# Kernel tuning notes

Measured on AMD Instinct MI355X. Metric: run time of the kernel, lower is better.

## Reference

```python
import math
import jax, jax.numpy as jnp
import numpy as np

STRATEGY = 'small'
K_PEAKS = 2
BW = math.radians(15.0)
HIGH_RATIO = 0.3
LOW_RATIO = 0.2
ALPHA = 1.2
BETA = 0.8
N_BINS = 180


def setup_inputs() -> dict:
    key = jax.random.key(0)
    k1, k2, k3 = jax.random.split(key, 3)
    x = jax.random.normal(k1, (16, 256, 128, 128), dtype=jnp.float32)
    w_in = jax.random.normal(k2, (16, 256), dtype=jnp.float32) * 0.06    # proj_in 1x1 conv weight [c_mid, C]
    w_out = jax.random.normal(k3, (256, 16), dtype=jnp.float32) * 0.25   # proj_out 1x1 conv weight [C, c_mid]
    return {"x": x, "w_in": w_in, "w_out": w_out}


def _forward(x, w_in, w_out):
    B, C, H, W = x.shape
    pi = jnp.float32(math.pi)
    cy, cx = H // 2, W // 2
    y = jnp.arange(H, dtype=jnp.float32)[:, None]
    xg = jnp.arange(W, dtype=jnp.float32)[None, :]
    r = jnp.sqrt((y - cy) ** 2 + (xg - cx) ** 2)                 # [H, W]
    theta = jnp.arctan2(y - cy, xg - cx) + pi                    # [H, W] in [0, 2pi]
    r_max = float(min(cy, cx))

    # 1x1 conv in
    x_proj = jnp.einsum('mc,bchw->bmhw', w_in, x)                # [B, c_mid, H, W]

    fs = jnp.fft.fftshift(jnp.fft.fft2(x_proj, norm='ortho'), axes=(-2, -1))
    mag = jnp.abs(fs)                                            # [B, c_mid, H, W]

    # ---- peak direction detection (180-bin angular histogram of high-freq energy) ----
    theta_mod = theta % pi
    high_mask = (r > HIGH_RATIO * r_max).astype(jnp.float32)     # [H, W]
    bin_edges = jnp.linspace(0.0, math.pi, N_BINS + 1, dtype=jnp.float32)
    mag_avg = mag.mean(axis=1)                                   # [B, H, W]
    weighted = (mag_avg * high_mask).reshape(B, -1)              # [B, H*W]
    bin_idx = jnp.clip(jnp.searchsorted(bin_edges, theta_mod.reshape(-1), side='left') - 1, 0, N_BINS - 1)
    energy = jax.vmap(lambda w: jax.ops.segment_sum(w, bin_idx, num_segments=N_BINS))(weighted)  # [B, 180]

    # smooth with [0.25, 0.5, 0.25], zero padding
    ep = jnp.pad(energy, ((0, 0), (1, 1)))
    es = 0.25 * ep[:, :-2] + 0.5 * ep[:, 1:-1] + 0.25 * ep[:, 2:]  # [B, 180]

    mean_e = es.mean(axis=-1, keepdims=True)
    is_peak = (es > mean_e) & (es > jnp.roll(es, 1, axis=-1)) & (es > jnp.roll(es, -1, axis=-1))
    vals = jnp.where(is_peak, es, -jnp.inf)
    topv, topi = jax.lax.top_k(vals, K_PEAKS)                    # [B, k]
    count = jnp.sum(topv > -jnp.inf, axis=-1)                    # [B] number of valid peaks (<= k)
    amax = jnp.argmax(es, axis=-1)                               # fallback when no peak found
    topi = jnp.where((count > 0)[:, None], topi, amax[:, None])
    eff = jnp.maximum(count, 1)
    pos = jnp.minimum(jnp.arange(K_PEAKS)[None, :], (eff - 1)[:, None])  # pad with last valid peak
    final_idx = jnp.take_along_axis(topi, pos, axis=1)           # [B, k]
    bin_center = (bin_edges[:-1] + bin_edges[1:]) * 0.5
    peak_angles = bin_center[final_idx]                          # [B, k]

    # ---- gain map (channel-independent) ----
    if STRATEGY == 'small':
        pa = peak_angles
        base_mask = high_mask
    else:
        pa = (peak_angles + pi / 2) % pi
        base_mask = (r <= LOW_RATIO * r_max).astype(jnp.float32)
    diff = jnp.abs(theta[None, None] - pa[:, :, None, None])     # [B, k, H, W]
    diff = jnp.minimum(diff, pi - diff)
    in_region = (diff <= BW) & (base_mask[None, None] > 0)
    enh = jnp.any(in_region, axis=1).astype(jnp.float32)         # [B, H, W]
    gain = jnp.where(enh > 0, jnp.float32(ALPHA), jnp.float32(1.0))
    other_high = high_mask[None] * (1.0 - enh)
    gain = gain * (1.0 - other_high) + other_high * BETA         # [B, H, W]

    fs_enh = fs * gain[:, None, :, :]
    x_enh = jnp.fft.ifft2(jnp.fft.ifftshift(fs_enh, axes=(-2, -1)), norm='ortho').real
    out = jnp.einsum('cm,bmhw->bchw', w_out, x_enh)
    return x + out


def reference(x, w_in, w_out):
    return _forward(x, w_in, w_out)
```

## Files before the change

kernel.cpp:

```cpp
#include <hip/hip_runtime.h>
#include <math.h>

#define NPX 16384

static constexpr float  PI_F   = 3.14159265358979323846f;
static constexpr double PI_D   = 3.14159265358979323846;
static constexpr double STEP_D = PI_D / 180.0;
static constexpr double BW_D   = 15.0 * (PI_D / 180.0);

typedef float f4 __attribute__((ext_vector_type(4)));
typedef float f2 __attribute__((ext_vector_type(2)));

__device__ __forceinline__ int swz(int r, int c) {
    return (r << 7) | (c ^ (r ^ (r >> 1)));
}
__device__ __forceinline__ int brev7(int x) { return (int)(__brev((unsigned)x) >> 25); }
__device__ __forceinline__ float2 cadd(float2 a, float2 b){ return make_float2(a.x+b.x, a.y+b.y); }
__device__ __forceinline__ float2 csub(float2 a, float2 b){ return make_float2(a.x-b.x, a.y-b.y); }
__device__ __forceinline__ float2 cmul(float2 a, float re, float im){
    return make_float2(a.x*re - a.y*im, a.x*im + a.y*re);
}
__device__ __forceinline__ double edge_d(int i) {
    return (i >= 180) ? PI_D : (double)i * STEP_D;
}

__global__ void k0_tables(double* __restrict__ theta_s, int* __restrict__ bin_s,
                          double* __restrict__ energy) {
    int p = blockIdx.x * blockDim.x + threadIdx.x;
    if (p < NPX) {
        int r = p >> 7, c = p & 127;
        int pix = ((brev7(r) ^ 64) << 7) | (brev7(c) ^ 64);
        int h = pix >> 7, w = pix & 127;
        double dy = (double)(h - 64), dx = (double)(w - 64);
        double theta = atan2(dy, dx) + PI_D;
        theta_s[p] = theta;
        double v = fmod(theta, PI_D);
        int cnt = 0;
        for (int i = 0; i <= 180; ++i) cnt += (edge_d(i) < v) ? 1 : 0;
        int bin = cnt - 1;
        if (bin < 0) bin = 0;
        if (bin > 179) bin = 179;
        int r2 = (h - 64)*(h - 64) + (w - 64)*(w - 64);
        bool high = (r2 >= 369);
        bin_s[p] = high ? bin : -1;
    }
    if (blockIdx.x == 0) {
        for (int i = threadIdx.x; i < 16 * 180; i += blockDim.x) energy[i] = 0.0;
    }
}

__global__ __launch_bounds__(256, 1) void k1_proj(const float* __restrict__ x,
        const float* __restrict__ w_in, float* __restrict__ xpp) {
    int b = blockIdx.y, z = blockIdx.z;
    int t4 = blockIdx.x * blockDim.x + threadIdx.x;
    const f4* xb = (const f4*)(x + ((size_t)b * 256 + (size_t)z * 128) * NPX);
    f4 acc[16];
    #pragma unroll
    for (int m = 0; m < 16; ++m) acc[m] = (f4)0.0f;
    #pragma unroll 16
    for (int c = 0; c < 128; ++c) {
        f4 xv = xb[(size_t)c * (NPX/4) + t4];
        #pragma unroll
        for (int m = 0; m < 16; ++m) {
            float wv = w_in[m * 256 + z * 128 + c];
            acc[m] += wv * xv;
        }
    }
    f4* xp = (f4*)xpp + ((size_t)z * 256 + b * 16) * (NPX/4);
    #pragma unroll
    for (int m = 0; m < 16; ++m) xp[(size_t)m * (NPX/4) + t4] = acc[m];
}

__global__ __launch_bounds__(1024) void k_fft_fwd(const float* __restrict__ xpp,
        float2* __restrict__ fs, const int* __restrict__ bin_s,
        double* __restrict__ energy) {
    extern __shared__ float2 lds[];
    __shared__ float twr[64], twi[64];
    __shared__ double histp[8][180];
    const int tid = threadIdx.x;
    const int img = blockIdx.x;
    if (tid < 64) {
        float ang = (float)tid * (PI_F / 64.0f);
        twr[tid] = cosf(ang);
        twi[tid] = sinf(ang);
    }
    if (tid < 180) {
        #pragma unroll
        for (int g = 0; g < 8; ++g) histp[g][tid] = 0.0;
    }
    const f4* s0 = (const f4*)xpp + (size_t)img * (NPX/4);
    const f4* s1 = (const f4*)xpp + (size_t)(256 + img) * (NPX/4);
    #pragma unroll
    for (int it = 0; it < 4; ++it) {
        int p4 = tid + it * 1024;
        f4 v = s0[p4] + s1[p4];
        int pb = p4 * 4;
        #pragma unroll
        for (int j = 0; j < 4; ++j) {
            int p = pb + j;
            lds[swz(p >> 7, p & 127)] = make_float2(v[j], 0.0f);
        }
    }
    __syncthreads();
    #pragma unroll
    for (int dim = 0; dim < 2; ++dim) {
        #pragma unroll
        for (int s = 0; s <= 4; s += 2) {
            const int q = 32 >> s;
            #pragma unroll
            for (int it = 0; it < 4; ++it) {
                int fb = tid + it * 1024;
                int o = fb & 127;
                int bfi = fb >> 7;
                int p = bfi & (q - 1);
                int g = bfi >> (5 - s);
                int P = g * (128 >> s) + p;
                int k1 = p << s;
                float tc = twr[k1],   ts = twi[k1];
                float uc = twr[2*k1], us = twi[2*k1];
                int e0, e1, e2, e3;
                if (dim == 0) { e0=swz(o,P); e1=swz(o,P+q); e2=swz(o,P+2*q); e3=swz(o,P+3*q); }
                else          { e0=swz(P,o); e1=swz(P+q,o); e2=swz(P+2*q,o); e3=swz(P+3*q,o); }
                float2 a = lds[e0], b = lds[e1], c = lds[e2], d = lds[e3];
                float2 u0 = cadd(a, c);
                float2 u1 = cmul(csub(a, c), tc, -ts);
                float2 v0 = cadd(b, d);
                float2 v1 = cmul(csub(b, d), -ts, -tc);
                lds[e0] = cadd(u0, v0);
                lds[e1] = cmul(csub(u0, v0), uc, -us);
                lds[e2] = cadd(u1, v1);
                lds[e3] = cmul(csub(u1, v1), uc, -us);
            }
            __syncthreads();
        }
        #pragma unroll
        for (int it = 0; it < 8; ++it) {
            int fb = tid + it * 1024;
            int o = fb & 127;
            int g = fb >> 7;
            int e0, e1;
            if (dim == 0) { e0 = swz(o, 2*g); e1 = swz(o, 2*g+1); }
            else          { e0 = swz(2*g, o); e1 = swz(2*g+1, o); }
            float2 a = lds[e0], b = lds[e1];
            lds[e0] = cadd(a, b);
            lds[e1] = csub(a, b);
        }
        __syncthreads();
    }
    float2* dst = fs + (size_t)img * NPX;
    const int bofs = (img >> 4) * 180;
    const int grp = tid >> 7;
    #pragma unroll
    for (int it = 0; it < 16; ++it) {
        int p = tid + it * 1024;
        int r = p >> 7, c = p & 127;
        float2 v = lds[swz(r, c)];
        dst[p] = v;
        int bh = bin_s[p];
        if (bh >= 0) {
            double m = sqrt((double)v.x * (double)v.x + (double)v.y * (double)v.y);
            atomicAdd(&histp[grp][bh], m);
        }
    }
    __syncthreads();
    if (tid < 180) {
        double s = 0.0;
        #pragma unroll
        for (int g = 0; g < 8; ++g) s += histp[g][tid];
        atomicAdd(&energy[bofs + tid], s);
    }
}

__global__ void k3_peaks(const double* __restrict__ energy, const double* __restrict__ theta_s,
                         const int* __restrict__ bin_s, float* __restrict__ gain_s) {
    __shared__ double e[180], es[180];
    __shared__ double pa[2];
    int b = blockIdx.x, tid = threadIdx.x;
    if (tid < 180) e[tid] = energy[b * 180 + tid];
    __syncthreads();
    if (tid < 180) {
        double l = (tid > 0)   ? e[tid-1] : 0.0;
        double r = (tid < 179) ? e[tid+1] : 0.0;
        es[tid] = 0.25*l + 0.5*e[tid] + 0.25*r;
    }
    __syncthreads();
    if (tid == 0) {
        double sum = 0.0;
        for (int i = 0; i < 180; ++i) sum += es[i];
        double mean = sum / 180.0;
        double v0 = -INFINITY, v1 = -INFINITY;
        int   i0 = -1, i1 = -1;
        for (int i = 0; i < 180; ++i) {
            double prev = es[(i + 179) % 180];
            double nxt  = es[(i + 1) % 180];
            bool pk = (es[i] > mean) && (es[i] > prev) && (es[i] > nxt);
            if (pk) {
                double v = es[i];
                if (v > v0)      { v1 = v0; i1 = i0; v0 = v; i0 = i; }
                else if (v > v1) { v1 = v;  i1 = i; }
            }
        }
        int idx0, idx1;
        if (i0 < 0) {
            double mv = es[0]; int mi = 0;
            for (int i = 1; i < 180; ++i) if (es[i] > mv) { mv = es[i]; mi = i; }
            idx0 = idx1 = mi;
        } else if (i1 < 0) { idx0 = idx1 = i0; }
        else               { idx0 = i0; idx1 = i1; }
        pa[0] = (edge_d(idx0) + edge_d(idx0 + 1)) * 0.5;
        pa[1] = (edge_d(idx1) + edge_d(idx1 + 1)) * 0.5;
    }
    __syncthreads();
    double pa0 = pa[0], pa1 = pa[1];
    for (int p = tid; p < NPX; p += blockDim.x) {
        double th = theta_s[p];
        bool high = bin_s[p] >= 0;
        double d0 = fabs(th - pa0); d0 = fmin(d0, PI_D - d0);
        double d1 = fabs(th - pa1); d1 = fmin(d1, PI_D - d1);
        bool enh = ((d0 <= BW_D) || (d1 <= BW_D)) && high;
        float g = enh ? 1.2f : (high ? 0.8f : 1.0f);
        gain_s[(size_t)b * NPX + p] = g * (1.0f / 16384.0f);
    }
}

__global__ __launch_bounds__(1024) void k_fft_inv(const float2* __restrict__ fs,
        const float* __restrict__ gain_s, float* __restrict__ xe) {
    extern __shared__ float2 lds[];
    __shared__ float twr[64], twi[64];
    const int tid = threadIdx.x;
    const int img = blockIdx.x;
    if (tid < 64) {
        float ang = (float)tid * (PI_F / 64.0f);
        twr[tid] = cosf(ang);
        twi[tid] = sinf(ang);
    }
    const f4* srcv = (const f4*)(fs + (size_t)img * NPX);
    const f2* gbv  = (const f2*)(gain_s + (size_t)(img >> 4) * NPX);
    #pragma unroll
    for (int it = 0; it < 8; ++it) {
        int q = tid + it * 1024;
        f4 v = srcv[q];
        f2 g = gbv[q];
        int p = q * 2;
        lds[swz(p >> 7, p & 127)]             = make_float2(v.x * g.x, v.y * g.x);
        lds[swz((p+1) >> 7, (p+1) & 127)]     = make_float2(v.z * g.y, v.w * g.y);
    }
    __syncthreads();
    #pragma unroll
    for (int dim = 0; dim < 2; ++dim) {
        #pragma unroll
        for (int it = 0; it < 8; ++it) {
            int fb = tid + it * 1024;
            int o = fb & 127;
            int g = fb >> 7;
            int e0, e1;
            if (dim == 0) { e0 = swz(o, 2*g); e1 = swz(o, 2*g+1); }
            else          { e0 = swz(2*g, o); e1 = swz(2*g+1, o); }
            float2 a = lds[e0], b = lds[e1];
            lds[e0] = cadd(a, b);
            lds[e1] = csub(a, b);
        }
        __syncthreads();
        #pragma unroll
        for (int s = 4; s >= 0; s -= 2) {
            const int q = 32 >> s;
            #pragma unroll
            for (int it = 0; it < 4; ++it) {
                int fb = tid + it * 1024;
                int o = fb & 127;
                int bfi = fb >> 7;
                int p = bfi & (q - 1);
                int g = bfi >> (5 - s);
                int P = g * (128 >> s) + p;
                int k1 = p << s;
                float tc = twr[k1],   ts = twi[k1];
                float uc = twr[2*k1], us = twi[2*k1];
                int e0, e1, e2, e3;
                if (dim == 0) { e0=swz(o,P); e1=swz(o,P+q); e2=swz(o,P+2*q); e3=swz(o,P+3*q); }
                else          { e0=swz(P,o); e1=swz(P+q,o); e2=swz(P+2*q,o); e3=swz(P+3*q,o); }
                float2 o0 = lds[e0], o1 = lds[e1], o2 = lds[e2], o3 = lds[e3];
                float2 t1 = cmul(o1, uc, us);
                float2 u0 = cadd(o0, t1);
                float2 v0 = csub(o0, t1);
                float2 t3 = cmul(o3, uc, us);
                float2 u1 = cadd(o2, t3);
                float2 v1 = csub(o2, t3);
                float2 ta = cmul(u1, tc, ts);
                float2 tb = cmul(v1, -ts, tc);
                lds[e0] = cadd(u0, ta);
                lds[e2] = csub(u0, ta);
                lds[e1] = cadd(v0, tb);
                lds[e3] = csub(v0, tb);
            }
            __syncthreads();
        }
    }
    float* dstx = xe + (size_t)img * NPX;
    #pragma unroll
    for (int it = 0; it < 16; ++it) {
        int p = tid + it * 1024;
        dstx[p] = lds[swz(p >> 7, p & 127)].x;
    }
}

__global__ __launch_bounds__(256, 1) void k5_out(const float* __restrict__ x,
        const float* __restrict__ w_out, const float* __restrict__ xe,
        float* __restrict__ out) {
    int b = blockIdx.z, ct = blockIdx.y, pt = blockIdx.x, t = threadIdx.x;
    int p4 = pt * 256 + t;
    const f4* xeb = (const f4*)(xe + (size_t)b * 16 * NPX);
    f4 xv[16];
    #pragma unroll
    for (int m = 0; m < 16; ++m) xv[m] = xeb[(size_t)m * (NPX/4) + p4];
    #pragma unroll 8
    for (int cc = 0; cc < 16; ++cc) {
        int c = ct * 16 + cc;
        size_t base = ((size_t)b * 256 + c) * NPX;
        f4 a = ((const f4*)(x + base))[p4];
        #pragma unroll
        for (int m = 0; m < 16; ++m) {
            float wv = w_out[c * 16 + m];
            a += wv * xv[m];
        }
        __builtin_nontemporal_store(a, (f4*)(out + base) + p4);
    }
}

extern "C" void kernel_launch(void* const* d_in, const int* in_sizes, int n_in,
                              void* d_out, int out_size, void* d_ws, size_t ws_size,
                              hipStream_t stream) {
    const float* x     = (const float*)d_in[0];
    const float* w_in  = (const float*)d_in[1];
    const float* w_out = (const float*)d_in[2];
    float* out = (float*)d_out;
    char* ws = (char*)d_ws;

    double* theta_s = (double*)(ws);
    int*    bin_s   = (int*)   (ws + 0x20000);
    double* energy  = (double*)(ws + 0x30000);
    float*  gain_s  = (float*) (ws + 0x40000);
    float*  xe      = (float*) (ws + 0x140000);
    float*  xpp = (float*)((char*)d_out + ((size_t)128 << 20));
    float2* fs  = (float2*)((char*)d_out + ((size_t)224 << 20));

    (void)hipFuncSetAttribute((const void*)k_fft_fwd,
            hipFuncAttributeMaxDynamicSharedMemorySize, 131072);
    (void)hipFuncSetAttribute((const void*)k_fft_inv,
            hipFuncAttributeMaxDynamicSharedMemorySize, 131072);

    k0_tables<<<dim3(64), dim3(256), 0, stream>>>(theta_s, bin_s, energy);
    k1_proj  <<<dim3(16, 16, 2), dim3(256), 0, stream>>>(x, w_in, xpp);
    k_fft_fwd<<<dim3(256), dim3(1024), 131072, stream>>>(xpp, fs, bin_s, energy);
    k3_peaks <<<dim3(16), dim3(256), 0, stream>>>(energy, theta_s, bin_s, gain_s);
    k_fft_inv<<<dim3(256), dim3(1024), 131072, stream>>>(fs, gain_s, xe);
    k5_out   <<<dim3(16, 16, 16), dim3(256), 0, stream>>>(x, w_out, xe, out);
}
```

Before: 253.3 us.

## Fuse forward FFT, peak detection and inverse FFT into one cooperative kernel

Merges the forward FFT, peak-finding/gain computation and inverse FFT into one cooperative kernel. A grid-wide sync after the histogram accumulation replaces the kernel boundary, and the spectrum stays in LDS, so the complex spectrum and gain map are no longer written to and read back from global memory. Each block recomputes the peaks for its batch redundantly. In exchange it relies on all 256 blocks of 1024 threads with 128KB LDS being co-resident, and it adds a grid barrier cost.

```diff
diff --git a/kernel.cpp b/kernel.cpp
--- a/kernel.cpp
+++ b/kernel.cpp
@@ -1,5 +1,8 @@
 #include <hip/hip_runtime.h>
+#include <hip/hip_cooperative_groups.h>
 #include <math.h>
+
+namespace cg = cooperative_groups;
 
 #define NPX 16384
 
@@ -71,12 +74,14 @@
     for (int m = 0; m < 16; ++m) xp[(size_t)m * (NPX/4) + t4] = acc[m];
 }
 
-__global__ __launch_bounds__(1024) void k_fft_fwd(const float* __restrict__ xpp,
-        float2* __restrict__ fs, const int* __restrict__ bin_s,
-        double* __restrict__ energy) {
+__global__ __launch_bounds__(1024) void k_fused(const float* __restrict__ xpp,
+        const int* __restrict__ bin_s, const double* __restrict__ theta_s,
+        double* __restrict__ energy, float* __restrict__ xe) {
     extern __shared__ float2 lds[];
     __shared__ float twr[64], twi[64];
     __shared__ double histp[8][180];
+    __shared__ double es[180];
+    __shared__ double pa[2];
     const int tid = threadIdx.x;
     const int img = blockIdx.x;
     if (tid < 64) {
@@ -147,15 +152,12 @@
         }
         __syncthreads();
     }
-    float2* dst = fs + (size_t)img * NPX;
     const int bofs = (img >> 4) * 180;
     const int grp = tid >> 7;
     #pragma unroll
     for (int it = 0; it < 16; ++it) {
         int p = tid + it * 1024;
-        int r = p >> 7, c = p & 127;
-        float2 v = lds[swz(r, c)];
-        dst[p] = v;
+        float2 v = lds[swz(p >> 7, p & 127)];
         int bh = bin_s[p];
         if (bh >= 0) {
             double m = sqrt((double)v.x * (double)v.x + (double)v.y * (double)v.y);
@@ -169,19 +171,13 @@
         for (int g = 0; g < 8; ++g) s += histp[g][tid];
         atomicAdd(&energy[bofs + tid], s);
     }
-}
-
-__global__ void k3_peaks(const double* __restrict__ energy, const double* __restrict__ theta_s,
-                         const int* __restrict__ bin_s, float* __restrict__ gain_s) {
-    __shared__ double e[180], es[180];
-    __shared__ double pa[2];
-    int b = blockIdx.x, tid = threadIdx.x;
-    if (tid < 180) e[tid] = energy[b * 180 + tid];
-    __syncthreads();
+    __threadfence();
+    cg::this_grid().sync();
     if (tid < 180) {
-        double l = (tid > 0)   ? e[tid-1] : 0.0;
-        double r = (tid < 179) ? e[tid+1] : 0.0;
-        es[tid] = 0.25*l + 0.5*e[tid] + 0.25*r;
+        int i = tid;
+        double l = (i > 0)   ? energy[bofs + i - 1] : 0.0;
+        double r = (i < 179) ? energy[bofs + i + 1] : 0.0;
+        es[i] = 0.25*l + 0.5*energy[bofs + i] + 0.25*r;
     }
     __syncthreads();
     if (tid == 0) {
@@ -212,38 +208,18 @@
     }
     __syncthreads();
     double pa0 = pa[0], pa1 = pa[1];
-    for (int p = tid; p < NPX; p += blockDim.x) {
+    #pragma unroll
+    for (int it = 0; it < 16; ++it) {
+        int p = tid + it * 1024;
         double th = theta_s[p];
         bool high = bin_s[p] >= 0;
         double d0 = fabs(th - pa0); d0 = fmin(d0, PI_D - d0);
         double d1 = fabs(th - pa1); d1 = fmin(d1, PI_D - d1);
         bool enh = ((d0 <= BW_D) || (d1 <= BW_D)) && high;
-        float g = enh ? 1.2f : (high ? 0.8f : 1.0f);
-        gain_s[(size_t)b * NPX + p] = g * (1.0f / 16384.0f);
-    }
-}
-
-__global__ __launch_bounds__(1024) void k_fft_inv(const float2* __restrict__ fs,
-        const float* __restrict__ gain_s, float* __restrict__ xe) {
-    extern __shared__ float2 lds[];
-    __shared__ float twr[64], twi[64];
-    const int tid = threadIdx.x;
-    const int img = blockIdx.x;
-    if (tid < 64) {
-        float ang = (float)tid * (PI_F / 64.0f);
-        twr[tid] = cosf(ang);
-        twi[tid] = sinf(ang);
-    }
-    const f4* srcv = (const f4*)(fs + (size_t)img * NPX);
-    const f2* gbv  = (const f2*)(gain_s + (size_t)(img >> 4) * NPX);
-    #pragma unroll
-    for (int it = 0; it < 8; ++it) {
-        int q = tid + it * 1024;
-        f4 v = srcv[q];
-        f2 g = gbv[q];
-        int p = q * 2;
-        lds[swz(p >> 7, p & 127)]             = make_float2(v.x * g.x, v.y * g.x);
-        lds[swz((p+1) >> 7, (p+1) & 127)]     = make_float2(v.z * g.y, v.w * g.y);
+        float g = (enh ? 1.2f : (high ? 0.8f : 1.0f)) * (1.0f / 16384.0f);
+        int e = swz(p >> 7, p & 127);
+        float2 v = lds[e];
+        lds[e] = make_float2(v.x * g, v.y * g);
     }
     __syncthreads();
     #pragma unroll
@@ -338,20 +314,19 @@
     double* theta_s = (double*)(ws);
     int*    bin_s   = (int*)   (ws + 0x20000);
     double* energy  = (double*)(ws + 0x30000);
-    float*  gain_s  = (float*) (ws + 0x40000);
     float*  xe      = (float*) (ws + 0x140000);
     float*  xpp = (float*)((char*)d_out + ((size_t)128 << 20));
-    float2* fs  = (float2*)((char*)d_out + ((size_t)224 << 20));
-
-    (void)hipFuncSetAttribute((const void*)k_fft_fwd,
-            hipFuncAttributeMaxDynamicSharedMemorySize, 131072);
-    (void)hipFuncSetAttribute((const void*)k_fft_inv,
+
+    (void)hipFuncSetAttribute((const void*)k_fused,
             hipFuncAttributeMaxDynamicSharedMemorySize, 131072);
 
     k0_tables<<<dim3(64), dim3(256), 0, stream>>>(theta_s, bin_s, energy);
     k1_proj  <<<dim3(16, 16, 2), dim3(256), 0, stream>>>(x, w_in, xpp);
-    k_fft_fwd<<<dim3(256), dim3(1024), 131072, stream>>>(xpp, fs, bin_s, energy);
-    k3_peaks <<<dim3(16), dim3(256), 0, stream>>>(energy, theta_s, bin_s, gain_s);
-    k_fft_inv<<<dim3(256), dim3(1024), 131072, stream>>>(fs, gain_s, xe);
+
+    void* args[] = { (void*)&xpp, (void*)&bin_s, (void*)&theta_s,
+                     (void*)&energy, (void*)&xe };
+    (void)hipLaunchCooperativeKernel((const void*)k_fused, dim3(256), dim3(1024),
+                                     args, 131072, stream);
+
     k5_out   <<<dim3(16, 16, 16), dim3(256), 0, stream>>>(x, w_out, xe, out);
 }
```

Measured after the change: 370.8 us. +46.4%, slower.

## Split FFT row pass into two halves to overlap global loads with LDS compute

Applied to the files above, without the earlier changes.

The forward and inverse FFT kernels now issue all global loads up front, then run the row-direction FFT on the first 64 rows while the second half's loads are still in flight, then on the second 64 rows, before the column pass. Lighter LDS barriers (waitcnt plus s_barrier) replace __syncthreads inside the row passes. The output projection kernel's grid is also remapped so consecutive blocks share the same pixel tile across channel tiles, which should improve L2 reuse of xe. This holds more loaded values in registers, which raises register pressure in 1024-thread blocks.

```diff
diff --git a/kernel.cpp b/kernel.cpp
--- a/kernel.cpp
+++ b/kernel.cpp
@@ -22,6 +22,98 @@
 }
 __device__ __forceinline__ double edge_d(int i) {
     return (i >= 180) ? PI_D : (double)i * STEP_D;
+}
+__device__ __forceinline__ void lds_barrier() {
+    asm volatile("s_waitcnt lgkmcnt(0)" ::: "memory");
+    __builtin_amdgcn_s_barrier();
+}
+
+__device__ __forceinline__ void row_fft_fwd(float2* lds, const float* twr,
+                                            const float* twi, int tid, int rbase) {
+    #pragma unroll
+    for (int s = 0; s <= 4; s += 2) {
+        const int q = 32 >> s;
+        #pragma unroll
+        for (int it = 0; it < 2; ++it) {
+            int fb = tid + it * 1024;
+            int o = rbase + (fb & 63);
+            int bfi = fb >> 6;
+            int p = bfi & (q - 1);
+            int g = bfi >> (5 - s);
+            int P = g * (128 >> s) + p;
+            int k1 = p << s;
+            float tc = twr[k1],   ts = twi[k1];
+            float uc = twr[2*k1], us = twi[2*k1];
+            int e0=swz(o,P), e1=swz(o,P+q), e2=swz(o,P+2*q), e3=swz(o,P+3*q);
+            float2 a = lds[e0], b = lds[e1], c = lds[e2], d = lds[e3];
+            float2 u0 = cadd(a, c);
+            float2 u1 = cmul(csub(a, c), tc, -ts);
+            float2 v0 = cadd(b, d);
+            float2 v1 = cmul(csub(b, d), -ts, -tc);
+            lds[e0] = cadd(u0, v0);
+            lds[e1] = cmul(csub(u0, v0), uc, -us);
+            lds[e2] = cadd(u1, v1);
+            lds[e3] = cmul(csub(u1, v1), uc, -us);
+        }
+        lds_barrier();
+    }
+    #pragma unroll
+    for (int it = 0; it < 4; ++it) {
+        int fb = tid + it * 1024;
+        int o = rbase + (fb & 63);
+        int g = fb >> 6;
+        int e0 = swz(o, 2*g), e1 = swz(o, 2*g+1);
+        float2 a = lds[e0], b = lds[e1];
+        lds[e0] = cadd(a, b);
+        lds[e1] = csub(a, b);
+    }
+    lds_barrier();
+}
+
+__device__ __forceinline__ void row_fft_inv(float2* lds, const float* twr,
+                                            const float* twi, int tid, int rbase) {
+    #pragma unroll
+    for (int it = 0; it < 4; ++it) {
+        int fb = tid + it * 1024;
+        int o = rbase + (fb & 63);
+        int g = fb >> 6;
+        int e0 = swz(o, 2*g), e1 = swz(o, 2*g+1);
+        float2 a = lds[e0], b = lds[e1];
+        lds[e0] = cadd(a, b);
+        lds[e1] = csub(a, b);
+    }
+    lds_barrier();
+    #pragma unroll
+    for (int s = 4; s >= 0; s -= 2) {
+        const int q = 32 >> s;
+        #pragma unroll
+        for (int it = 0; it < 2; ++it) {
+            int fb = tid + it * 1024;
+            int o = rbase + (fb & 63);
+            int bfi = fb >> 6;
+            int p = bfi & (q - 1);
+            int g = bfi >> (5 - s);
+            int P = g * (128 >> s) + p;
+            int k1 = p << s;
+            float tc = twr[k1],   ts = twi[k1];
+            float uc = twr[2*k1], us = twi[2*k1];
+            int e0=swz(o,P), e1=swz(o,P+q), e2=swz(o,P+2*q), e3=swz(o,P+3*q);
+            float2 o0 = lds[e0], o1 = lds[e1], o2 = lds[e2], o3 = lds[e3];
+            float2 t1 = cmul(o1, uc, us);
+            float2 u0 = cadd(o0, t1);
+            float2 v0 = csub(o0, t1);
+            float2 t3 = cmul(o3, uc, us);
+            float2 u1 = cadd(o2, t3);
+            float2 v1 = csub(o2, t3);
+            float2 ta = cmul(u1, tc, ts);
+            float2 tb = cmul(v1, -ts, tc);
+            lds[e0] = cadd(u0, ta);
+            lds[e2] = csub(u0, ta);
+            lds[e1] = cadd(v0, tb);
+            lds[e3] = csub(v0, tb);
+        }
+        lds_barrier();
+    }
 }
 
 __global__ void k0_tables(double* __restrict__ theta_s, int* __restrict__ bin_s,
@@ -90,71 +182,85 @@
     }
     const f4* s0 = (const f4*)xpp + (size_t)img * (NPX/4);
     const f4* s1 = (const f4*)xpp + (size_t)(256 + img) * (NPX/4);
-    #pragma unroll
-    for (int it = 0; it < 4; ++it) {
-        int p4 = tid + it * 1024;
-        f4 v = s0[p4] + s1[p4];
-        int pb = p4 * 4;
+    f4 a00 = s0[tid],        a01 = s1[tid];
+    f4 a10 = s0[tid + 1024], a11 = s1[tid + 1024];
+    f4 b00 = s0[tid + 2048], b01 = s1[tid + 2048];
+    f4 b10 = s0[tid + 3072], b11 = s1[tid + 3072];
+    {
+        f4 va0 = a00 + a01, va1 = a10 + a11;
         #pragma unroll
         for (int j = 0; j < 4; ++j) {
-            int p = pb + j;
-            lds[swz(p >> 7, p & 127)] = make_float2(v[j], 0.0f);
-        }
-    }
-    __syncthreads();
-    #pragma unroll
-    for (int dim = 0; dim < 2; ++dim) {
-        #pragma unroll
-        for (int s = 0; s <= 4; s += 2) {
-            const int q = 32 >> s;
-            #pragma unroll
-            for (int it = 0; it < 4; ++it) {
-                int fb = tid + it * 1024;
-                int o = fb & 127;
-                int bfi = fb >> 7;
-                int p = bfi & (q - 1);
-                int g = bfi >> (5 - s);
-                int P = g * (128 >> s) + p;
-                int k1 = p << s;
-                float tc = twr[k1],   ts = twi[k1];
-                float uc = twr[2*k1], us = twi[2*k1];
-                int e0, e1, e2, e3;
-                if (dim == 0) { e0=swz(o,P); e1=swz(o,P+q); e2=swz(o,P+2*q); e3=swz(o,P+3*q); }
-                else          { e0=swz(P,o); e1=swz(P+q,o); e2=swz(P+2*q,o); e3=swz(P+3*q,o); }
-                float2 a = lds[e0], b = lds[e1], c = lds[e2], d = lds[e3];
-                float2 u0 = cadd(a, c);
-                float2 u1 = cmul(csub(a, c), tc, -ts);
-                float2 v0 = cadd(b, d);
-                float2 v1 = cmul(csub(b, d), -ts, -tc);
-                lds[e0] = cadd(u0, v0);
-                lds[e1] = cmul(csub(u0, v0), uc, -us);
-                lds[e2] = cadd(u1, v1);
-                lds[e3] = cmul(csub(u1, v1), uc, -us);
-            }
-            __syncthreads();
-        }
-        #pragma unroll
-        for (int it = 0; it < 8; ++it) {
+            int p = 4 * tid + j;
+            lds[swz(p >> 7, p & 127)] = make_float2(va0[j], 0.0f);
+        }
+        #pragma unroll
+        for (int j = 0; j < 4; ++j) {
+            int p = 4 * (tid + 1024) + j;
+            lds[swz(p >> 7, p & 127)] = make_float2(va1[j], 0.0f);
+        }
+    }
+    lds_barrier();
+    row_fft_fwd(lds, twr, twi, tid, 0);
+    {
+        f4 vb0 = b00 + b01, vb1 = b10 + b11;
+        #pragma unroll
+        for (int j = 0; j < 4; ++j) {
+            int p = 4 * (tid + 2048) + j;
+            lds[swz(p >> 7, p & 127)] = make_float2(vb0[j], 0.0f);
+        }
+        #pragma unroll
+        for (int j = 0; j < 4; ++j) {
+            int p = 4 * (tid + 3072) + j;
+            lds[swz(p >> 7, p & 127)] = make_float2(vb1[j], 0.0f);
+        }
+    }
+    lds_barrier();
+    row_fft_fwd(lds, twr, twi, tid, 64);
+    #pragma unroll
+    for (int s = 0; s <= 4; s += 2) {
+        const int q = 32 >> s;
+        #pragma unroll
+        for (int it = 0; it < 4; ++it) {
             int fb = tid + it * 1024;
             int o = fb & 127;
-            int g = fb >> 7;
-            int e0, e1;
-            if (dim == 0) { e0 = swz(o, 2*g); e1 = swz(o, 2*g+1); }
-            else          { e0 = swz(2*g, o); e1 = swz(2*g+1, o); }
-            float2 a = lds[e0], b = lds[e1];
-            lds[e0] = cadd(a, b);
-            lds[e1] = csub(a, b);
+            int bfi = fb >> 7;
+            int p = bfi & (q - 1);
+            int g = bfi >> (5 - s);
+            int P = g * (128 >> s) + p;
+            int k1 = p << s;
+            float tc = twr[k1],   ts = twi[k1];
+            float uc = twr[2*k1], us = twi[2*k1];
+            int e0=swz(P,o), e1=swz(P+q,o), e2=swz(P+2*q,o), e3=swz(P+3*q,o);
+            float2 a = lds[e0], b = lds[e1], c = lds[e2], d = lds[e3];
+            float2 u0 = cadd(a, c);
+            float2 u1 = cmul(csub(a, c), tc, -ts);
+            float2 v0 = cadd(b, d);
+            float2 v1 = cmul(csub(b, d), -ts, -tc);
+            lds[e0] = cadd(u0, v0);
+            lds[e1] = cmul(csub(u0, v0), uc, -us);
+            lds[e2] = cadd(u1, v1);
+            lds[e3] = cmul(csub(u1, v1), uc, -us);
         }
         __syncthreads();
     }
+    #pragma unroll
+    for (int it = 0; it < 8; ++it) {
+        int fb = tid + it * 1024;
+        int o = fb & 127;
+        int g = fb >> 7;
+        int e0 = swz(2*g, o), e1 = swz(2*g+1, o);
+        float2 a = lds[e0], b = lds[e1];
+        lds[e0] = cadd(a, b);
+        lds[e1] = csub(a, b);
+    }
+    __syncthreads();
     float2* dst = fs + (size_t)img * NPX;
     const int bofs = (img >> 4) * 180;
     const int grp = tid >> 7;
     #pragma unroll
     for (int it = 0; it < 16; ++it) {
         int p = tid + it * 1024;
-        int r = p >> 7, c = p & 127;
-        float2 v = lds[swz(r, c)];
+        float2 v = lds[swz(p >> 7, p & 127)];
         dst[p] = v;
         int bh = bin_s[p];
         if (bh >= 0) {
@@ -236,64 +342,67 @@
     }
     const f4* srcv = (const f4*)(fs + (size_t)img * NPX);
     const f2* gbv  = (const f2*)(gain_s + (size_t)(img >> 4) * NPX);
+    f4 a0 = srcv[tid],        a1 = srcv[tid + 1024];
+    f4 a2 = srcv[tid + 2048], a3 = srcv[tid + 3072];
+    f2 g0 = gbv[tid],         g1 = gbv[tid + 1024];
+    f2 g2 = gbv[tid + 2048],  g3 = gbv[tid + 3072];
+    f4 b0 = srcv[tid + 4096], b1 = srcv[tid + 5120];
+    f4 b2 = srcv[tid + 6144], b3 = srcv[tid + 7168];
+    f2 h0 = gbv[tid + 4096],  h1 = gbv[tid + 5120];
+    f2 h2 = gbv[tid + 6144],  h3 = gbv[tid + 7168];
+    #define PUT2(vv, gg, qq) { int p = (qq) * 2;                                      \
+        lds[swz(p >> 7, p & 127)]         = make_float2(vv.x * gg.x, vv.y * gg.x);    \
+        lds[swz((p+1) >> 7, (p+1) & 127)] = make_float2(vv.z * gg.y, vv.w * gg.y); }
+    PUT2(a0, g0, tid)        PUT2(a1, g1, tid + 1024)
+    PUT2(a2, g2, tid + 2048) PUT2(a3, g3, tid + 3072)
+    lds_barrier();
+    row_fft_inv(lds, twr, twi, tid, 0);
+    PUT2(b0, h0, tid + 4096) PUT2(b1, h1, tid + 5120)
+    PUT2(b2, h2, tid + 6144) PUT2(b3, h3, tid + 7168)
+    lds_barrier();
+    row_fft_inv(lds, twr, twi, tid, 64);
+    #undef PUT2
     #pragma unroll
     for (int it = 0; it < 8; ++it) {
-        int q = tid + it * 1024;
-        f4 v = srcv[q];
-        f2 g = gbv[q];
-        int p = q * 2;
-        lds[swz(p >> 7, p & 127)]             = make_float2(v.x * g.x, v.y * g.x);
-        lds[swz((p+1) >> 7, (p+1) & 127)]     = make_float2(v.z * g.y, v.w * g.y);
-    }
-    __syncthreads();
-    #pragma unroll
-    for (int dim = 0; dim < 2; ++dim) {
-        #pragma unroll
-        for (int it = 0; it < 8; ++it) {
+        int fb = tid + it * 1024;
+        int o = fb & 127;
+        int g = fb >> 7;
+        int e0 = swz(2*g, o), e1 = swz(2*g+1, o);
+        float2 a = lds[e0], b = lds[e1];
+        lds[e0] = cadd(a, b);
+        lds[e1] = csub(a, b);
+    }
+    __syncthreads();
+    #pragma unroll
+    for (int s = 4; s >= 0; s -= 2) {
+        const int q = 32 >> s;
+        #pragma unroll
+        for (int it = 0; it < 4; ++it) {
             int fb = tid + it * 1024;
             int o = fb & 127;
-            int g = fb >> 7;
-            int e0, e1;
-            if (dim == 0) { e0 = swz(o, 2*g); e1 = swz(o, 2*g+1); }
-            else          { e0 = swz(2*g, o); e1 = swz(2*g+1, o); }
-            float2 a = lds[e0], b = lds[e1];
-            lds[e0] = cadd(a, b);
-            lds[e1] = csub(a, b);
+            int bfi = fb >> 7;
+            int p = bfi & (q - 1);
+            int g = bfi >> (5 - s);
+            int P = g * (128 >> s) + p;
+            int k1 = p << s;
+            float tc = twr[k1],   ts = twi[k1];
+            float uc = twr[2*k1], us = twi[2*k1];
+            int e0=swz(P,o), e1=swz(P+q,o), e2=swz(P+2*q,o), e3=swz(P+3*q,o);
+            float2 o0 = lds[e0], o1 = lds[e1], o2 = lds[e2], o3 = lds[e3];
+            float2 t1 = cmul(o1, uc, us);
+            float2 u0 = cadd(o0, t1);
+            float2 v0 = csub(o0, t1);
+            float2 t3 = cmul(o3, uc, us);
+            float2 u1 = cadd(o2, t3);
+            float2 v1 = csub(o2, t3);
+            float2 ta = cmul(u1, tc, ts);
+            float2 tb = cmul(v1, -ts, tc);
+            lds[e0] = cadd(u0, ta);
+            lds[e2] = csub(u0, ta);
+            lds[e1] = cadd(v0, tb);
+            lds[e3] = csub(v0, tb);
         }
         __syncthreads();
-        #pragma unroll
-        for (int s = 4; s >= 0; s -= 2) {
-            const int q = 32 >> s;
-            #pragma unroll
-            for (int it = 0; it < 4; ++it) {
-                int fb = tid + it * 1024;
-                int o = fb & 127;
-                int bfi = fb >> 7;
-                int p = bfi & (q - 1);
-                int g = bfi >> (5 - s);
-                int P = g * (128 >> s) + p;
-                int k1 = p << s;
-                float tc = twr[k1],   ts = twi[k1];
-                float uc = twr[2*k1], us = twi[2*k1];
-                int e0, e1, e2, e3;
-                if (dim == 0) { e0=swz(o,P); e1=swz(o,P+q); e2=swz(o,P+2*q); e3=swz(o,P+3*q); }
-                else          { e0=swz(P,o); e1=swz(P+q,o); e2=swz(P+2*q,o); e3=swz(P+3*q,o); }
-                float2 o0 = lds[e0], o1 = lds[e1], o2 = lds[e2], o3 = lds[e3];
-                float2 t1 = cmul(o1, uc, us);
-                float2 u0 = cadd(o0, t1);
-                float2 v0 = csub(o0, t1);
-                float2 t3 = cmul(o3, uc, us);
-                float2 u1 = cadd(o2, t3);
-                float2 v1 = csub(o2, t3);
-                float2 ta = cmul(u1, tc, ts);
-                float2 tb = cmul(v1, -ts, tc);
-                lds[e0] = cadd(u0, ta);
-                lds[e2] = csub(u0, ta);
-                lds[e1] = cadd(v0, tb);
-                lds[e3] = csub(v0, tb);
-            }
-            __syncthreads();
-        }
     }
     float* dstx = xe + (size_t)img * NPX;
     #pragma unroll
@@ -306,7 +415,9 @@
 __global__ __launch_bounds__(256, 1) void k5_out(const float* __restrict__ x,
         const float* __restrict__ w_out, const float* __restrict__ xe,
         float* __restrict__ out) {
-    int b = blockIdx.z, ct = blockIdx.y, pt = blockIdx.x, t = threadIdx.x;
+    int bx = blockIdx.x;
+    int ct = bx & 15, pt = bx >> 4;
+    int b = blockIdx.z, t = threadIdx.x;
     int p4 = pt * 256 + t;
     const f4* xeb = (const f4*)(xe + (size_t)b * 16 * NPX);
     f4 xv[16];
@@ -353,5 +464,5 @@
     k_fft_fwd<<<dim3(256), dim3(1024), 131072, stream>>>(xpp, fs, bin_s, energy);
     k3_peaks <<<dim3(16), dim3(256), 0, stream>>>(energy, theta_s, bin_s, gain_s);
     k_fft_inv<<<dim3(256), dim3(1024), 131072, stream>>>(fs, gain_s, xe);
-    k5_out   <<<dim3(16, 16, 16), dim3(256), 0, stream>>>(x, w_out, xe, out);
-}
+    k5_out   <<<dim3(256, 1, 16), dim3(256), 0, stream>>>(x, w_out, xe, out);
+}
```

Result: slower. 262.5 us (+3.6%).
